# Optimization experiments

Measured on AMD Instinct MI355X. Metric: run time of the kernel, lower is better.

## Reference

```python
import jax, jax.numpy as jnp
import numpy as np

OUT, IN = 4096, 4096      # weight_shape
VDIM = 8                  # codebook vector_dim
CODEBOOK_SIZE = 256
LEVEL = 2                 # haar_decomposition_level
INV_SQRT2 = 0.7071067811865476


def unpack_bool(packed, shape):
    # packed: int array of bytes (values 0..255); unpack 8 bits per byte (LSB first)
    bits = (packed[:, None] >> jnp.arange(8, dtype=packed.dtype)) & 1  # [n_bytes, 8]
    return bits.reshape(shape)


def inverse_haar(c, level):
    # c: [..., n] orthonormal Haar coefficients laid out [a_L, d_L, d_{L-1}, ..., d_1]
    n = c.shape[-1]
    m = n >> level
    a = c[..., :m]
    while m < n:
        d = c[..., m:2 * m]
        even = (a + d) * INV_SQRT2
        odd = (a - d) * INV_SQRT2
        a = jnp.stack([even, odd], axis=-1).reshape(c.shape[:-1] + (2 * m,))
        m *= 2
    return a


def setup_inputs() -> dict:
    key = jax.random.key(0)
    k1, k2, k3, k4, k5 = jax.random.split(key, 5)
    x = jax.random.normal(k1, (4, 2048, IN), dtype=jnp.float32)
    codebook = jax.random.normal(k2, (CODEBOOK_SIZE, VDIM), dtype=jnp.float32)
    scales = jax.random.uniform(k5, (OUT, 1), dtype=jnp.float32)
    indices = jax.random.randint(k3, (OUT * IN // VDIM,), 0, CODEBOOK_SIZE, dtype=jnp.int32)
    signs_packed = jax.random.randint(k4, (OUT * IN // 8,), 0, 256, dtype=jnp.int32)
    return {"x": x, "codebook": codebook, "scales": scales,
            "indices": indices, "signs_packed": signs_packed}


def reference(x, codebook, scales, indices, signs_packed):
    # codebook gather -> haar-domain magnitudes, reshaped to signs_shape = weight shape
    haar_freq = codebook[indices].reshape(OUT, IN)
    # unpack sign bits and map {0,1} -> {-1,+1}
    signs = 2.0 * unpack_bool(signs_packed, (OUT, IN)).astype(haar_freq.dtype) - 1.0
    haar_freq = haar_freq * signs
    # multi-level inverse Haar wavelet along in_features
    w = inverse_haar(haar_freq, LEVEL)
    w = w * scales  # per-output-row scales
    return jnp.einsum('bsi,oi->bso', x, w)
```

## Files before the change

### kernel.cpp

```cpp
#include <hip/hip_runtime.h>
#include <hip/hip_bf16.h>

typedef unsigned short u16;
typedef unsigned int u32;
typedef float f32x4 __attribute__((ext_vector_type(4)));
typedef u16 u16x4 __attribute__((ext_vector_type(4)));
typedef u16 u16x8 __attribute__((ext_vector_type(8)));
typedef __bf16 bf16x8 __attribute__((ext_vector_type(8)));

#define OUT_DIM 4096
#define IN_DIM  4096
#define M_DIM   8192

__device__ __forceinline__ u16 f2bf(float f) {
  u32 u = __builtin_bit_cast(u32, f);
  return (u16)((u + 0x7FFFu + ((u >> 16) & 1u)) >> 16);
}

__global__ __launch_bounds__(256) void build_w_kernel(
    const float* __restrict__ codebook, const float* __restrict__ scales,
    const int* __restrict__ indices, const int* __restrict__ signs,
    u16* __restrict__ W) {
  __shared__ float c[IN_DIM];
  const int o   = blockIdx.x;
  const int tid = threadIdx.x;
  for (int g = tid; g < IN_DIM / 8; g += 256) {
    const int idx = indices[o * (IN_DIM / 8) + g];
    const int sp  = signs[o * (IN_DIM / 8) + g];
    f32x4 c0 = *(const f32x4*)&codebook[idx * 8];
    f32x4 c1 = *(const f32x4*)&codebook[idx * 8 + 4];
    float v[8] = {c0[0], c0[1], c0[2], c0[3], c1[0], c1[1], c1[2], c1[3]};
#pragma unroll
    for (int j = 0; j < 8; ++j)
      c[g * 8 + j] = ((sp >> j) & 1) ? v[j] : -v[j];
  }
  __syncthreads();
  const float scale = scales[o];
  const float S = 0.70710678118654752440f;
  for (int t = tid; t < IN_DIM / 4; t += 256) {
    float a   = c[t];
    float d1  = c[IN_DIM / 4 + t];
    float d2a = c[IN_DIM / 2 + 2 * t];
    float d2b = c[IN_DIM / 2 + 2 * t + 1];
    float e  = (a + d1) * S;
    float od = (a - d1) * S;
    u16x4 w;
    w[0] = f2bf((e  + d2a) * S * scale);
    w[1] = f2bf((e  - d2a) * S * scale);
    w[2] = f2bf((od + d2b) * S * scale);
    w[3] = f2bf((od - d2b) * S * scale);
    *(u16x4*)&W[(size_t)o * IN_DIM + 4 * t] = w;
  }
}

__global__ __launch_bounds__(256) void cvt_x_kernel(
    const float* __restrict__ X, u16* __restrict__ Xb) {
  const int stride = gridDim.x * blockDim.x;
  const int n8 = (M_DIM * IN_DIM) / 8;
  for (int i = blockIdx.x * blockDim.x + threadIdx.x; i < n8; i += stride) {
    f32x4 a = *(const f32x4*)&X[(size_t)i * 8];
    f32x4 b = *(const f32x4*)&X[(size_t)i * 8 + 4];
    u16x8 r;
    r[0] = f2bf(a[0]); r[1] = f2bf(a[1]); r[2] = f2bf(a[2]); r[3] = f2bf(a[3]);
    r[4] = f2bf(b[0]); r[5] = f2bf(b[1]); r[6] = f2bf(b[2]); r[7] = f2bf(b[3]);
    *(u16x8*)&Xb[(size_t)i * 8] = r;
  }
}

__global__ __launch_bounds__(512, 2) void gemm_bt_kernel(
    const u16* __restrict__ A,
    const u16* __restrict__ B,
    float*     __restrict__ C) {
  constexpr int K    = IN_DIM;
  constexpr int NT   = K / 32;
  constexpr int BUFB = 32768;
  extern __shared__ char smem[];

  const int tid  = threadIdx.x;
  const int wave = tid >> 6;
  const int lane = tid & 63;

  const int swz = (blockIdx.x & 7) * 64 + (blockIdx.x >> 3);
  const int bm = (swz >> 4) * 256;
  const int bn = (swz & 15) * 256;

  const int wr  = (wave >> 2) * 128;
  const int wc  = (wave & 3) * 64;
  const int fr  = lane & 15;
  const int fkB = (lane >> 4) * 16;

  int offA[8], offB[4];
#pragma unroll
  for (int h = 0; h < 8; ++h) {
    int o = (wr + h * 16 + fr) * 64 + fkB;
    offA[h] = o ^ ((o >> 3) & 0x30);
  }
#pragma unroll
  for (int n = 0; n < 4; ++n) {
    int o = (wc + n * 16 + fr) * 64 + fkB;
    offB[n] = 16384 + (o ^ ((o >> 3) & 0x30));
  }

  const u16* srcA[2]; const u16* srcB[2];
#pragma unroll
  for (int i = 0; i < 2; ++i) {
    int d = i * 8192 + tid * 16;
    int l = d ^ ((d >> 3) & 0x30);
    int row = d >> 6;
    srcA[i] = A + (size_t)(bm + row) * K + ((l & 63) >> 1);
    srcB[i] = B + (size_t)(bn + row) * K + ((l & 63) >> 1);
  }
  const int ldsW = wave * 1024;

  auto stage = [&](int tt) {
    char* base = smem + (tt & 3) * BUFB + ldsW;
#pragma unroll
    for (int i = 0; i < 2; ++i) {
      __builtin_amdgcn_global_load_lds(
          (const __attribute__((address_space(1))) void*)(srcA[i] + tt * 32),
          (__attribute__((address_space(3))) void*)(base + i * 8192), 16, 0, 0);
      __builtin_amdgcn_global_load_lds(
          (const __attribute__((address_space(1))) void*)(srcB[i] + tt * 32),
          (__attribute__((address_space(3))) void*)(base + 16384 + i * 8192), 16, 0, 0);
    }
  };

  f32x4 acc[8][4] = {};
  bf16x8 aX[8], bX[4], aY[8], bY[4];

  stage(0); stage(1); stage(2);
  asm volatile("s_waitcnt vmcnt(8)" ::: "memory");
  __builtin_amdgcn_s_barrier();
  {
    const char* buf0 = smem;
#pragma unroll
    for (int n = 0; n < 4; ++n) bX[n] = *(const bf16x8*)(buf0 + offB[n]);
#pragma unroll
    for (int m = 0; m < 8; ++m) aX[m] = *(const bf16x8*)(buf0 + offA[m]);
  }

  auto tileStep = [&](int t, bf16x8 (&cA)[8], bf16x8 (&cB)[4],
                      bf16x8 (&nA)[8], bf16x8 (&nB)[4]) {
    if (t + 3 < NT) stage(t + 3);
    if (t + 3 < NT)       asm volatile("s_waitcnt vmcnt(8)" ::: "memory");
    else if (t + 3 == NT) asm volatile("s_waitcnt vmcnt(4)" ::: "memory");
    else if (t + 2 == NT) asm volatile("s_waitcnt vmcnt(0)" ::: "memory");
    __builtin_amdgcn_s_barrier();
    if (t + 1 < NT) {
      const char* bufn = smem + ((t + 1) & 3) * BUFB;
#pragma unroll
      for (int n = 0; n < 4; ++n) nB[n] = *(const bf16x8*)(bufn + offB[n]);
#pragma unroll
      for (int m = 0; m < 8; ++m) nA[m] = *(const bf16x8*)(bufn + offA[m]);
    }
    __builtin_amdgcn_s_setprio(1);
#pragma unroll
    for (int m = 0; m < 8; ++m)
#pragma unroll
      for (int n = 0; n < 4; ++n)
        acc[m][n] = __builtin_amdgcn_mfma_f32_16x16x32_bf16(cA[m], cB[n], acc[m][n], 0, 0, 0);
    __builtin_amdgcn_s_setprio(0);
    __builtin_amdgcn_s_barrier();
  };

  for (int t = 0; t < NT; t += 2) {
    tileStep(t,     aX, bX, aY, bY);
    tileStep(t + 1, aY, bY, aX, bX);
  }

#pragma unroll
  for (int h = 0; h < 8; ++h)
#pragma unroll
    for (int n = 0; n < 4; ++n) {
      const int col = bn + wc + n * 16 + fr;
#pragma unroll
      for (int j = 0; j < 4; ++j) {
        const int row = bm + wr + h * 16 + (lane >> 4) * 4 + j;
        C[(size_t)row * OUT_DIM + col] = acc[h][n][j];
      }
    }
}

extern "C" void kernel_launch(void* const* d_in, const int* in_sizes, int n_in,
                              void* d_out, int out_size, void* d_ws, size_t ws_size,
                              hipStream_t stream) {
  const float* x        = (const float*)d_in[0];
  const float* codebook = (const float*)d_in[1];
  const float* scales   = (const float*)d_in[2];
  const int*   indices  = (const int*)d_in[3];
  const int*   signs    = (const int*)d_in[4];
  float* out = (float*)d_out;

  u16* W  = (u16*)d_ws;
  u16* Xb = (u16*)d_ws + (size_t)OUT_DIM * IN_DIM;

  (void)hipFuncSetAttribute((const void*)gemm_bt_kernel,
                            hipFuncAttributeMaxDynamicSharedMemorySize, 131072);

  build_w_kernel<<<OUT_DIM, 256, 0, stream>>>(codebook, scales, indices, signs, W);
  cvt_x_kernel<<<2048, 256, 0, stream>>>(x, Xb);
  gemm_bt_kernel<<<(M_DIM / 256) * (OUT_DIM / 256), 512, 131072, stream>>>(Xb, W, out);
}
```

Measured before the change: 305.8 us.

## Restructure GEMM main loop into eight-phase ping-pong schedule with split staging

The GEMM main loop now works on 64-wide K tiles held in two 64KB buffers. Each tile is split into phases covering one K half and one M quarter. Within each phase it does fine-grained global-to-LDS staging, a small LDS fragment read, and 16 MFMAs, with barriers between phases. The goal is to overlap loads and LDS reads with compute at a finer grain and to cut register pressure, so occupancy is set to one 512-thread block per CU. The trade-off is more barriers per tile, lower occupancy, and fragments that are no longer double-buffered in registers, since LDS reads now wait on lgkmcnt(0) right before each MFMA block.

```diff
diff --git a/kernel.cpp b/kernel.cpp
--- a/kernel.cpp
+++ b/kernel.cpp
@@ -67,13 +67,13 @@
   }
 }
 
-__global__ __launch_bounds__(512, 2) void gemm_bt_kernel(
+__global__ __launch_bounds__(512, 1) void gemm_bt_kernel(
     const u16* __restrict__ A,
     const u16* __restrict__ B,
     float*     __restrict__ C) {
-  constexpr int K    = IN_DIM;
-  constexpr int NT   = K / 32;
-  constexpr int BUFB = 32768;
+  constexpr int K   = IN_DIM;
+  constexpr int NT  = K / 64;
+  constexpr int NIT = NT / 2;
   extern __shared__ char smem[];
 
   const int tid  = threadIdx.x;
@@ -89,84 +89,92 @@
   const int fr  = lane & 15;
   const int fkB = (lane >> 4) * 16;
 
-  int offA[8], offB[4];
-#pragma unroll
-  for (int h = 0; h < 8; ++h) {
-    int o = (wr + h * 16 + fr) * 64 + fkB;
-    offA[h] = o ^ ((o >> 3) & 0x30);
-  }
+  int offA[2][4], offB[4];
+#pragma unroll
+  for (int mq = 0; mq < 2; ++mq)
+#pragma unroll
+    for (int m = 0; m < 4; ++m) {
+      int o = (wr + mq * 64 + m * 16 + fr) * 64 + fkB;
+      offA[mq][m] = o ^ ((o >> 3) & 0x30);
+    }
 #pragma unroll
   for (int n = 0; n < 4; ++n) {
     int o = (wc + n * 16 + fr) * 64 + fkB;
     offB[n] = 16384 + (o ^ ((o >> 3) & 0x30));
   }
 
-  const u16* srcA[2]; const u16* srcB[2];
-#pragma unroll
-  for (int i = 0; i < 2; ++i) {
-    int d = i * 8192 + tid * 16;
-    int l = d ^ ((d >> 3) & 0x30);
-    int row = d >> 6;
-    srcA[i] = A + (size_t)(bm + row) * K + ((l & 63) >> 1);
-    srcB[i] = B + (size_t)(bn + row) * K + ((l & 63) >> 1);
-  }
+  const int d0 = tid * 16,        d1 = 8192 + tid * 16;
+  const int l0 = d0 ^ ((d0 >> 3) & 0x30), l1 = d1 ^ ((d1 >> 3) & 0x30);
+  const u16* srcA0 = A + (size_t)(bm + (d0 >> 6)) * K + ((l0 & 63) >> 1);
+  const u16* srcA1 = A + (size_t)(bm + (d1 >> 6)) * K + ((l1 & 63) >> 1);
+  const u16* srcB0 = B + (size_t)(bn + (d0 >> 6)) * K + ((l0 & 63) >> 1);
+  const u16* srcB1 = B + (size_t)(bn + (d1 >> 6)) * K + ((l1 & 63) >> 1);
   const int ldsW = wave * 1024;
 
-  auto stage = [&](int tt) {
-    char* base = smem + (tt & 3) * BUFB + ldsW;
-#pragma unroll
-    for (int i = 0; i < 2; ++i) {
-      __builtin_amdgcn_global_load_lds(
-          (const __attribute__((address_space(1))) void*)(srcA[i] + tt * 32),
-          (__attribute__((address_space(3))) void*)(base + i * 8192), 16, 0, 0);
-      __builtin_amdgcn_global_load_lds(
-          (const __attribute__((address_space(1))) void*)(srcB[i] + tt * 32),
-          (__attribute__((address_space(3))) void*)(base + 16384 + i * 8192), 16, 0, 0);
-    }
+#define GLD(SRC, DST)                                              \
+  __builtin_amdgcn_global_load_lds(                                \
+      (const __attribute__((address_space(1))) void*)(SRC),        \
+      (__attribute__((address_space(3))) void*)(DST), 16, 0, 0)
+
+  auto stagePart = [&](int bufi, int ks, int part, int tile) {
+    char* base = smem + bufi * 65536 + ks * 32768 + part * 16384 + ldsW;
+    const u16* s0 = (part ? srcB0 : srcA0) + tile * 64 + ks * 32;
+    const u16* s1 = (part ? srcB1 : srcA1) + tile * 64 + ks * 32;
+    GLD(s0, base);
+    GLD(s1, base + 8192);
   };
 
   f32x4 acc[8][4] = {};
-  bf16x8 aX[8], bX[4], aY[8], bY[4];
-
-  stage(0); stage(1); stage(2);
-  asm volatile("s_waitcnt vmcnt(8)" ::: "memory");
+  bf16x8 aq[4], bq[4];
+
+  stagePart(0, 0, 0, 0); stagePart(0, 0, 1, 0);
+  stagePart(0, 1, 0, 0); stagePart(0, 1, 1, 0);
+  stagePart(1, 0, 0, 1); stagePart(1, 0, 1, 1);
+  asm volatile("s_waitcnt vmcnt(4)" ::: "memory");
   __builtin_amdgcn_s_barrier();
-  {
-    const char* buf0 = smem;
-#pragma unroll
-    for (int n = 0; n < 4; ++n) bX[n] = *(const bf16x8*)(buf0 + offB[n]);
-#pragma unroll
-    for (int m = 0; m < 8; ++m) aX[m] = *(const bf16x8*)(buf0 + offA[m]);
-  }
-
-  auto tileStep = [&](int t, bf16x8 (&cA)[8], bf16x8 (&cB)[4],
-                      bf16x8 (&nA)[8], bf16x8 (&nB)[4]) {
-    if (t + 3 < NT) stage(t + 3);
-    if (t + 3 < NT)       asm volatile("s_waitcnt vmcnt(8)" ::: "memory");
-    else if (t + 3 == NT) asm volatile("s_waitcnt vmcnt(4)" ::: "memory");
-    else if (t + 2 == NT) asm volatile("s_waitcnt vmcnt(0)" ::: "memory");
-    __builtin_amdgcn_s_barrier();
-    if (t + 1 < NT) {
-      const char* bufn = smem + ((t + 1) & 3) * BUFB;
-#pragma unroll
-      for (int n = 0; n < 4; ++n) nB[n] = *(const bf16x8*)(bufn + offB[n]);
-#pragma unroll
-      for (int m = 0; m < 8; ++m) nA[m] = *(const bf16x8*)(bufn + offA[m]);
-    }
-    __builtin_amdgcn_s_setprio(1);
-#pragma unroll
-    for (int m = 0; m < 8; ++m)
-#pragma unroll
-      for (int n = 0; n < 4; ++n)
-        acc[m][n] = __builtin_amdgcn_mfma_f32_16x16x32_bf16(cA[m], cB[n], acc[m][n], 0, 0, 0);
-    __builtin_amdgcn_s_setprio(0);
-    __builtin_amdgcn_s_barrier();
-  };
-
-  for (int t = 0; t < NT; t += 2) {
-    tileStep(t,     aX, bX, aY, bY);
-    tileStep(t + 1, aY, bY, aX, bX);
-  }
+
+#define PHASE(BUFI, KS, MQ, READB, STAGE, GATE)                              \
+  {                                                                          \
+    const char* rb = smem + (BUFI) * 65536 + (KS) * 32768;                   \
+    if (READB) {                                                             \
+      _Pragma("unroll")                                                      \
+      for (int n = 0; n < 4; ++n) bq[n] = *(const bf16x8*)(rb + offB[n]);    \
+    }                                                                        \
+    _Pragma("unroll")                                                        \
+    for (int m = 0; m < 4; ++m) aq[m] = *(const bf16x8*)(rb + offA[MQ][m]);  \
+    STAGE;                                                                   \
+    __builtin_amdgcn_s_barrier();                                            \
+    asm volatile("s_waitcnt lgkmcnt(0)" ::: "memory");                       \
+    __builtin_amdgcn_s_setprio(1);                                           \
+    _Pragma("unroll")                                                        \
+    for (int m = 0; m < 4; ++m)                                              \
+      _Pragma("unroll")                                                      \
+      for (int n = 0; n < 4; ++n)                                            \
+        acc[(MQ) * 4 + m][n] = __builtin_amdgcn_mfma_f32_16x16x32_bf16(      \
+            aq[m], bq[n], acc[(MQ) * 4 + m][n], 0, 0, 0);                    \
+    __builtin_amdgcn_s_setprio(0);                                           \
+    GATE;                                                                    \
+    __builtin_amdgcn_s_barrier();                                            \
+  }
+
+  for (int i = 0; i < NIT; ++i) {
+    const int t0 = 2 * i;
+    const bool more = (i < NIT - 1);
+    PHASE(0, 0, 0, 1, stagePart(1, 1, 0, t0 + 1), )
+    PHASE(0, 0, 1, 0, stagePart(1, 1, 1, t0 + 1), )
+    PHASE(0, 1, 0, 1, if (more) stagePart(0, 0, 0, t0 + 2), )
+    PHASE(0, 1, 1, 0, if (more) stagePart(0, 0, 1, t0 + 2),
+          if (more) { asm volatile("s_waitcnt vmcnt(4)" ::: "memory"); }
+          else      { asm volatile("s_waitcnt vmcnt(0)" ::: "memory"); })
+    PHASE(1, 0, 0, 1, if (more) stagePart(0, 1, 0, t0 + 2), )
+    PHASE(1, 0, 1, 0, if (more) stagePart(0, 1, 1, t0 + 2), )
+    PHASE(1, 1, 0, 1, if (more) stagePart(1, 0, 0, t0 + 3), )
+    PHASE(1, 1, 1, 0, if (more) stagePart(1, 0, 1, t0 + 3),
+          if (more) { asm volatile("s_waitcnt vmcnt(4)" ::: "memory"); }
+          else      { asm volatile("s_waitcnt vmcnt(0)" ::: "memory"); })
+  }
+#undef PHASE
+#undef GLD
 
 #pragma unroll
   for (int h = 0; h < 8; ++h)
```

Measured after the change: 286.0 us. -6.5%, faster.
